# Performance work log

Hardware: AMD Instinct MI355X
Metric: run time of the kernel (lower is better)

Reference implementation:

```python
import jax, jax.numpy as jnp
import numpy as np

S, T, B, V, E, H = 64, 48, 32, 32000, 512, 512


def setup_inputs() -> dict:
    key = jax.random.key(0)
    ks = jax.random.split(key, 24)
    def n(k, shape, s=0.05):
        return jax.random.normal(k, shape, dtype=jnp.float32) * s
    return {
        "src": jax.random.randint(ks[0], (S, B), 0, V),
        "trg": jax.random.randint(ks[1], (T, B), 0, V),
        "enc_emb": n(ks[2], (V, E)),
        "enc_Wih0": n(ks[3], (3 * H, E)),
        "enc_Whh0": n(ks[4], (3 * H, H)),
        "enc_bih0": n(ks[5], (3 * H,)),
        "enc_bhh0": n(ks[6], (3 * H,)),
        "enc_Wih1": n(ks[7], (3 * H, H)),
        "enc_Whh1": n(ks[8], (3 * H, H)),
        "enc_bih1": n(ks[9], (3 * H,)),
        "enc_bhh1": n(ks[10], (3 * H,)),
        "dec_emb": n(ks[11], (V, E)),
        "dec_Wih0": n(ks[12], (3 * H, E)),
        "dec_Whh0": n(ks[13], (3 * H, H)),
        "dec_bih0": n(ks[14], (3 * H,)),
        "dec_bhh0": n(ks[15], (3 * H,)),
        "dec_Wih1": n(ks[16], (3 * H, H)),
        "dec_Whh1": n(ks[17], (3 * H, H)),
        "dec_bih1": n(ks[18], (3 * H,)),
        "dec_bhh1": n(ks[19], (3 * H,)),
        "out_W": n(ks[20], (V, H)),
        "out_b": n(ks[21], (V,)),
    }


def gru_layer(xs, h0, Wih, Whh, bih, bhh):
    """PyTorch-convention GRU over a (T, B, D) sequence. Returns (ys, h_T)."""
    def step(h, x):
        gi = x @ Wih.T + bih          # (B, 3H)
        gh = h @ Whh.T + bhh          # (B, 3H)
        ir, iz, inn = jnp.split(gi, 3, axis=-1)
        hr, hz, hn = jnp.split(gh, 3, axis=-1)
        r = jax.nn.sigmoid(ir + hr)
        z = jax.nn.sigmoid(iz + hz)
        cand = jnp.tanh(inn + r * hn)
        h_new = (1.0 - z) * cand + z * h
        return h_new, h_new
    hT, ys = jax.lax.scan(step, h0, xs)
    return ys, hT


def reference(src, trg, enc_emb, enc_Wih0, enc_Whh0, enc_bih0, enc_bhh0,
              enc_Wih1, enc_Whh1, enc_bih1, enc_bhh1,
              dec_emb, dec_Wih0, dec_Whh0, dec_bih0, dec_bhh0,
              dec_Wih1, dec_Whh1, dec_bih1, dec_bhh1, out_W, out_b):
    b = src.shape[1]
    h = enc_Whh0.shape[1]
    h0 = jnp.zeros((b, h), dtype=enc_emb.dtype)
    # Encoder: 2-layer unidirectional GRU (dropout=0, eval mode)
    x = enc_emb[src]                                   # (S, B, E)
    y0, h0_f = gru_layer(x, h0, enc_Wih0, enc_Whh0, enc_bih0, enc_bhh0)
    _, h1_f = gru_layer(y0, h0, enc_Wih1, enc_Whh1, enc_bih1, enc_bhh1)
    # decoder_hidden = encoder_hidden[-2:] -> (layer0 final, layer1 final)
    # Decoder with teacher_forcing_ratio = 1.0: inputs are trg[:-1]
    d = dec_emb[trg[:-1]]                              # (T-1, B, E)
    d0, _ = gru_layer(d, h0_f, dec_Wih0, dec_Whh0, dec_bih0, dec_bhh0)
    d1, _ = gru_layer(d0, h1_f, dec_Wih1, dec_Whh1, dec_bih1, dec_bhh1)
    logits = d1 @ out_W.T + out_b                      # (T-1, B, V)
    return logits
```

## Files before the change

### kernel.cpp

```cpp
#include <hip/hip_runtime.h>
#include <hip/hip_bf16.h>

typedef __bf16 bf16x8 __attribute__((ext_vector_type(8)));
typedef float  f32x4  __attribute__((ext_vector_type(4)));

__device__ __forceinline__ void store_bf8(__bf16* dst, float4 a, float4 b) {
  bf16x8 v;
  v[0] = (__bf16)a.x; v[1] = (__bf16)a.y; v[2] = (__bf16)a.z; v[3] = (__bf16)a.w;
  v[4] = (__bf16)b.x; v[5] = (__bf16)b.y; v[6] = (__bf16)b.z; v[7] = (__bf16)b.w;
  *(bf16x8*)dst = v;
}

__device__ __forceinline__ bf16x8 load_coh16(const __bf16* p) {
  union { unsigned long long u[2]; bf16x8 v; } r;
  r.u[0] = __hip_atomic_load((const unsigned long long*)p,     __ATOMIC_RELAXED, __HIP_MEMORY_SCOPE_AGENT);
  r.u[1] = __hip_atomic_load((const unsigned long long*)p + 1, __ATOMIC_RELAXED, __HIP_MEMORY_SCOPE_AGENT);
  return r.v;
}

__device__ __forceinline__ void store_coh16B(__bf16* p, bf16x8 v) {
  asm volatile("global_store_dwordx4 %0, %1, off sc0 sc1"
               :: "v"(p), "v"(v) : "memory");
}

__device__ __forceinline__ void wait_flags(const unsigned* f, unsigned tgt) {
  const unsigned* p = f + (threadIdx.x & 31) * 32;
  for (;;) {
    const unsigned v = __hip_atomic_load(p, __ATOMIC_RELAXED, __HIP_MEMORY_SCOPE_AGENT);
    if (__all((int)(v >= tgt))) break;
    __builtin_amdgcn_s_sleep(1);
  }
}

__global__ __launch_bounds__(256) void cvt_f32_bf16(
    const float* __restrict__ s, __bf16* __restrict__ d, long n8)
{
  long i = (long)blockIdx.x * 256 + threadIdx.x;
  if (i >= n8) return;
  const float4* sp = (const float4*)s + i * 2;
  store_bf8(d + i * 8, sp[0], sp[1]);
}

__global__ __launch_bounds__(64) void gather_cvt(
    const float* __restrict__ emb, const int* __restrict__ idx, __bf16* __restrict__ dst)
{
  const int r = blockIdx.x;
  const long row = idx[r];
  const float4* sp = (const float4*)(emb + row * 512) + threadIdx.x * 2;
  store_bf8(dst + (long)r * 512 + threadIdx.x * 8, sp[0], sp[1]);
}

__global__ __launch_bounds__(256) void gemm_bt(
    const __bf16* __restrict__ A, const __bf16* __restrict__ B,
    const float* __restrict__ bias, float* __restrict__ C, int M, int N)
{
  const int wave = threadIdx.x >> 6;
  const int lane = threadIdx.x & 63;
  const int l16 = lane & 15;
  const int quad = lane >> 4;

  const int m0 = blockIdx.x * 128 + wave * 32;
  const int n0 = blockIdx.y * 128;

  int r0 = m0 + l16;       if (r0 >= M) r0 = M - 1;
  int r1 = m0 + 16 + l16;  if (r1 >= M) r1 = M - 1;
  const __bf16* __restrict__ A0 = A + (long)r0 * 512 + quad * 8;
  const __bf16* __restrict__ A1 = A + (long)r1 * 512 + quad * 8;

  const __bf16* bp[8];
#pragma unroll
  for (int i = 0; i < 8; ++i)
    bp[i] = B + (long)(n0 + i * 16 + l16) * 512 + quad * 8;

  f32x4 acc[2][8];
#pragma unroll
  for (int mi = 0; mi < 2; ++mi)
#pragma unroll
    for (int i = 0; i < 8; ++i) acc[mi][i] = (f32x4){0.f, 0.f, 0.f, 0.f};

#pragma unroll
  for (int ks = 0; ks < 16; ++ks) {
    bf16x8 a0 = *(const bf16x8*)(A0 + ks * 32);
    bf16x8 a1 = *(const bf16x8*)(A1 + ks * 32);
#pragma unroll
    for (int i = 0; i < 8; ++i) {
      bf16x8 b = *(const bf16x8*)(bp[i] + ks * 32);
      acc[0][i] = __builtin_amdgcn_mfma_f32_16x16x32_bf16(a0, b, acc[0][i], 0, 0, 0);
      acc[1][i] = __builtin_amdgcn_mfma_f32_16x16x32_bf16(a1, b, acc[1][i], 0, 0, 0);
    }
  }

#pragma unroll
  for (int mi = 0; mi < 2; ++mi) {
    const int crow = m0 + mi * 16 + quad * 4;
#pragma unroll
    for (int i = 0; i < 8; ++i) {
      const int n = n0 + i * 16 + l16;
      const float bv = bias ? bias[n] : 0.0f;
#pragma unroll
      for (int r = 0; r < 4; ++r) {
        const int row = crow + r;
        if (row < M) C[(long)row * N + n] = acc[mi][i][r] + bv;
      }
    }
  }
}

__global__ __launch_bounds__(128) void gru2_pipe(
    const float* __restrict__ GI,
    const float* __restrict__ Whh0, const float* __restrict__ bhh0,
    const float* __restrict__ Wih1, const float* __restrict__ bih1,
    const float* __restrict__ Whh1, const float* __restrict__ bhh1,
    __bf16* __restrict__ Y0, __bf16* __restrict__ Y1,
    const __bf16* __restrict__ h0i, const __bf16* __restrict__ h1i,
    float* __restrict__ hf0, float* __restrict__ hf1,
    unsigned* __restrict__ flags0, unsigned* __restrict__ flags1, int T)
{
  __shared__ __align__(16) __bf16 wh[48 * 520];
  __shared__ __align__(16) __bf16 wi[48 * 520];
  __shared__ __align__(16) __bf16 hlds[32][16];

  const int tid = threadIdx.x;
  const int L   = blockIdx.x >> 5;
  const int c   = blockIdx.x & 31;
  const int w   = tid >> 6;
  const int lane = tid & 63;
  const int l16 = lane & 15;
  const int quad = lane >> 4;

  const float* __restrict__ Whh = L ? Whh1 : Whh0;
  const float* __restrict__ bhh = L ? bhh1 : bhh0;
  __bf16* __restrict__ Yown = L ? Y1 : Y0;
  const __bf16* __restrict__ hini = L ? h1i : h0i;
  float* __restrict__ hf = L ? hf1 : hf0;
  unsigned* __restrict__ fOwn = L ? flags1 : flags0;

  for (int ch = tid; ch < 48 * 64; ch += 128) {
    const int lr = ch >> 6, kc = ch & 63;
    const int g = lr >> 4, j = lr & 15;
    const float4* sp = (const float4*)(Whh + (long)(g * 512 + c * 16 + j) * 512) + kc * 2;
    store_bf8(&wh[lr * 520 + kc * 8], sp[0], sp[1]);
  }
  if (L) {
    for (int ch = tid; ch < 48 * 64; ch += 128) {
      const int lr = ch >> 6, kc = ch & 63;
      const int g = lr >> 4, j = lr & 15;
      const float4* sp = (const float4*)(Wih1 + (long)(g * 512 + c * 16 + j) * 512) + kc * 2;
      store_bf8(&wi[lr * 520 + kc * 8], sp[0], sp[1]);
    }
  }

  float bR = bhh[0 * 512 + c * 16 + l16];
  float bZ = bhh[1 * 512 + c * 16 + l16];
  float bH = bhh[2 * 512 + c * 16 + l16];
  float bN = 0.f;
  if (L) {
    bR += bih1[0 * 512 + c * 16 + l16];
    bZ += bih1[1 * 512 + c * 16 + l16];
    bN  = bih1[2 * 512 + c * 16 + l16];
  }
  __syncthreads();

  const int b0  = w * 16 + quad * 4;
  const int col = c * 16 + l16;

  float hprev[4];
#pragma unroll
  for (int r = 0; r < 4; ++r) hprev[r] = hf[(b0 + r) * 512 + col];

  for (int t = 0; t < T; ++t) {
    float giR[4] = {0, 0, 0, 0}, giZ[4] = {0, 0, 0, 0}, giN[4] = {0, 0, 0, 0};
    if (!L) {
      const float* GIt = GI + (long)t * 49152;
#pragma unroll
      for (int r = 0; r < 4; ++r) {
        const float* gp = GIt + (b0 + r) * 1536 + col;
        giR[r] = gp[0];
        giZ[r] = gp[512];
        giN[r] = gp[1024];
      }
    }

    f32x4 accR = {bR, bR, bR, bR};
    f32x4 accZ = {bZ, bZ, bZ, bZ};
    f32x4 accH = {bH, bH, bH, bH};
    f32x4 accN = {bN, bN, bN, bN};

    if (L) {
      wait_flags(flags0, (unsigned)(t + 1));
      const __bf16* xA = Y0 + (long)(t + 1) * 16384 + (w * 16 + l16) * 512 + quad * 8;
      bf16x8 xa[16];
#pragma unroll
      for (int ks = 0; ks < 16; ++ks) xa[ks] = load_coh16(xA + ks * 32);
#pragma unroll
      for (int ks = 0; ks < 16; ++ks) {
        const int o = ks * 32 + quad * 8;
        accR = __builtin_amdgcn_mfma_f32_16x16x32_bf16(xa[ks], *(const bf16x8*)&wi[(     l16) * 520 + o], accR, 0, 0, 0);
        accZ = __builtin_amdgcn_mfma_f32_16x16x32_bf16(xa[ks], *(const bf16x8*)&wi[(16 + l16) * 520 + o], accZ, 0, 0, 0);
        accN = __builtin_amdgcn_mfma_f32_16x16x32_bf16(xa[ks], *(const bf16x8*)&wi[(32 + l16) * 520 + o], accN, 0, 0, 0);
      }
      if (t) wait_flags(flags1, (unsigned)t);
    } else if (t) {
      wait_flags(flags0, (unsigned)t);
    }

    const __bf16* hsrc = t ? (Yown + (long)t * 16384) : hini;
    const __bf16* hA = hsrc + (w * 16 + l16) * 512 + quad * 8;
    bf16x8 ha[16];
#pragma unroll
    for (int ks = 0; ks < 16; ++ks) ha[ks] = load_coh16(hA + ks * 32);
#pragma unroll
    for (int ks = 0; ks < 16; ++ks) {
      const int o = ks * 32 + quad * 8;
      accR = __builtin_amdgcn_mfma_f32_16x16x32_bf16(ha[ks], *(const bf16x8*)&wh[(     l16) * 520 + o], accR, 0, 0, 0);
      accZ = __builtin_amdgcn_mfma_f32_16x16x32_bf16(ha[ks], *(const bf16x8*)&wh[(16 + l16) * 520 + o], accZ, 0, 0, 0);
      accH = __builtin_amdgcn_mfma_f32_16x16x32_bf16(ha[ks], *(const bf16x8*)&wh[(32 + l16) * 520 + o], accH, 0, 0, 0);
    }

#pragma unroll
    for (int r = 0; r < 4; ++r) {
      float rs = accR[r], zs = accZ[r], hn = accH[r], nn = accN[r];
      if (!L) { rs += giR[r]; zs += giZ[r]; nn = giN[r]; }
      const float rg = __fdividef(1.0f, 1.0f + __expf(-rs));
      const float zg = __fdividef(1.0f, 1.0f + __expf(-zs));
      const float a2 = nn + rg * hn;
      const float e2 = __expf(2.0f * a2);
      const float cand = 1.0f - __fdividef(2.0f, e2 + 1.0f);
      const float hnew = (1.0f - zg) * cand + zg * hprev[r];
      hprev[r] = hnew;
      hlds[b0 + r][l16] = (__bf16)hnew;
    }
    __syncthreads();

    __bf16* yout = Yown + (long)(t + 1) * 16384;
    if (tid < 64) {
      const int row = tid >> 1, half = tid & 1;
      bf16x8 hv = *(const bf16x8*)&hlds[row][half * 8];
      store_coh16B(yout + (long)row * 512 + c * 16 + half * 8, hv);
    }
    asm volatile("s_waitcnt vmcnt(0)" ::: "memory");
    __syncthreads();
    if (tid == 0)
      __hip_atomic_store(fOwn + c * 32, (unsigned)(t + 1),
                         __ATOMIC_RELAXED, __HIP_MEMORY_SCOPE_AGENT);
  }

#pragma unroll
  for (int r = 0; r < 4; ++r) hf[(b0 + r) * 512 + col] = hprev[r];
}

extern "C" void kernel_launch(void* const* d_in, const int* in_sizes, int n_in,
                              void* d_out, int out_size, void* d_ws, size_t ws_size,
                              hipStream_t stream)
{
  const int* src = (const int*)d_in[0];
  const int* trg = (const int*)d_in[1];
  const float* enc_emb  = (const float*)d_in[2];
  const float* enc_Wih0 = (const float*)d_in[3];
  const float* enc_Whh0 = (const float*)d_in[4];
  const float* enc_bih0 = (const float*)d_in[5];
  const float* enc_bhh0 = (const float*)d_in[6];
  const float* enc_Wih1 = (const float*)d_in[7];
  const float* enc_Whh1 = (const float*)d_in[8];
  const float* enc_bih1 = (const float*)d_in[9];
  const float* enc_bhh1 = (const float*)d_in[10];
  const float* dec_emb  = (const float*)d_in[11];
  const float* dec_Wih0 = (const float*)d_in[12];
  const float* dec_Whh0 = (const float*)d_in[13];
  const float* dec_bih0 = (const float*)d_in[14];
  const float* dec_bhh0 = (const float*)d_in[15];
  const float* dec_Wih1 = (const float*)d_in[16];
  const float* dec_Whh1 = (const float*)d_in[17];
  const float* dec_bih1 = (const float*)d_in[18];
  const float* dec_bhh1 = (const float*)d_in[19];
  const float* out_W    = (const float*)d_in[20];
  const float* out_b    = (const float*)d_in[21];

  char* ws = (char*)d_ws;
  float*  GI    = (float*)(ws + 0);
  __bf16* Xenc  = (__bf16*)(ws + 12582912);
  __bf16* Xdec  = (__bf16*)(ws + 14680064);
  __bf16* Y0e   = (__bf16*)(ws + 16220160);
  __bf16* Y1e   = (__bf16*)(ws + 18350080);
  __bf16* Y0d   = (__bf16*)(ws + 20480000);
  __bf16* Y1d   = (__bf16*)(ws + 22052864);
  __bf16* Wb0   = (__bf16*)(ws + 23625728);
  __bf16* Wb2   = (__bf16*)(ws + 25198592);
  __bf16* outWb = (__bf16*)(ws + 26771456);
  float*  hf0   = (float*)(ws + 59539456);
  float*  hf1   = (float*)(ws + 59604992);
  __bf16* zb    = (__bf16*)(ws + 59670528);
  unsigned* flags = (unsigned*)(ws + 59703296);

  hipMemsetAsync(hf0, 0, 131072, stream);
  hipMemsetAsync(zb, 0, 32768, stream);
  hipMemsetAsync(flags, 0, 16384, stream);

  gather_cvt<<<2048, 64, 0, stream>>>(enc_emb, src, Xenc);
  gather_cvt<<<1504, 64, 0, stream>>>(dec_emb, trg, Xdec);
  cvt_f32_bf16<<<384, 256, 0, stream>>>(enc_Wih0, Wb0, 98304);
  cvt_f32_bf16<<<384, 256, 0, stream>>>(dec_Wih0, Wb2, 98304);
  cvt_f32_bf16<<<8000, 256, 0, stream>>>(out_W, outWb, 2048000);

  gemm_bt<<<dim3(16, 12), 256, 0, stream>>>(Xenc, Wb0, enc_bih0, GI, 2048, 1536);
  gru2_pipe<<<64, 128, 0, stream>>>(GI, enc_Whh0, enc_bhh0,
                                    enc_Wih1, enc_bih1, enc_Whh1, enc_bhh1,
                                    Y0e, Y1e, zb, zb, hf0, hf1,
                                    flags + 0, flags + 1024, 64);
  gemm_bt<<<dim3(12, 12), 256, 0, stream>>>(Xdec, Wb2, dec_bih0, GI, 1504, 1536);
  gru2_pipe<<<64, 128, 0, stream>>>(GI, dec_Whh0, dec_bhh0,
                                    dec_Wih1, dec_bih1, dec_Whh1, dec_bhh1,
                                    Y0d, Y1d, Y0e + 64 * 16384, Y1e + 64 * 16384, hf0, hf1,
                                    flags + 2048, flags + 3072, 47);

  gemm_bt<<<dim3(12, 250), 256, 0, stream>>>(Y1d + 16384, outWb, out_b,
                                             (float*)d_out, 1504, 32000);
}
```

Baseline: 1.299 ms.

## Stage GEMM tiles in LDS with swizzle and per-wave GRU sync flags

The GEMM is rewritten to stage 128x64 A/B tiles in shared memory with an XOR swizzle, register prefetch of the next K slab, and a 1-D grid with an XCD-aware block remap. Separately, the GRU pipeline drops block-wide barriers in favour of per-wave flags, so each wave waits only on the matching batch half. Its coherent atomic loads become plain vector loads, and h is stored with per-lane dwordx2. The plain loads after relaxed flag polling may read stale data across workgroups, which risks correctness in exchange for lower sync and load overhead.

New measurement: 1.235 ms. 1.05x faster.

```diff
diff --git a/kernel.cpp b/kernel.cpp
--- a/kernel.cpp
+++ b/kernel.cpp
@@ -11,25 +11,14 @@
   *(bf16x8*)dst = v;
 }
 
-__device__ __forceinline__ bf16x8 load_coh16(const __bf16* p) {
-  union { unsigned long long u[2]; bf16x8 v; } r;
-  r.u[0] = __hip_atomic_load((const unsigned long long*)p,     __ATOMIC_RELAXED, __HIP_MEMORY_SCOPE_AGENT);
-  r.u[1] = __hip_atomic_load((const unsigned long long*)p + 1, __ATOMIC_RELAXED, __HIP_MEMORY_SCOPE_AGENT);
-  return r.v;
-}
-
-__device__ __forceinline__ void store_coh16B(__bf16* p, bf16x8 v) {
-  asm volatile("global_store_dwordx4 %0, %1, off sc0 sc1"
-               :: "v"(p), "v"(v) : "memory");
-}
-
-__device__ __forceinline__ void wait_flags(const unsigned* f, unsigned tgt) {
-  const unsigned* p = f + (threadIdx.x & 31) * 32;
+__device__ __forceinline__ void wait_flags_w(const unsigned* f, int w, unsigned tgt) {
+  const unsigned* p = f + ((((threadIdx.x & 31) << 1) + w) << 5);
   for (;;) {
     const unsigned v = __hip_atomic_load(p, __ATOMIC_RELAXED, __HIP_MEMORY_SCOPE_AGENT);
     if (__all((int)(v >= tgt))) break;
     __builtin_amdgcn_s_sleep(1);
   }
+  asm volatile("" ::: "memory");
 }
 
 __global__ __launch_bounds__(256) void cvt_f32_bf16(
@@ -50,27 +39,38 @@
   store_bf8(dst + (long)r * 512 + threadIdx.x * 8, sp[0], sp[1]);
 }
 
-__global__ __launch_bounds__(256) void gemm_bt(
+__global__ __launch_bounds__(256) void gemm_tile(
     const __bf16* __restrict__ A, const __bf16* __restrict__ B,
-    const float* __restrict__ bias, float* __restrict__ C, int M, int N)
-{
-  const int wave = threadIdx.x >> 6;
-  const int lane = threadIdx.x & 63;
-  const int l16 = lane & 15;
+    const float* __restrict__ bias, float* __restrict__ C,
+    int M, int N, int NT)
+{
+  __shared__ __align__(16) __bf16 sA[128 * 64];
+  __shared__ __align__(16) __bf16 sB[128 * 64];
+
+  const int nwg = gridDim.x;
+  const int bid = blockIdx.x;
+  const int swz = (nwg & 7) ? bid : ((bid & 7) * (nwg >> 3) + (bid >> 3));
+  const int m0 = (swz / NT) * 128;
+  const int n0 = (swz % NT) * 128;
+
+  const int tid  = threadIdx.x;
+  const int wave = tid >> 6;
+  const int lane = tid & 63;
+  const int l16  = lane & 15;
   const int quad = lane >> 4;
 
-  const int m0 = blockIdx.x * 128 + wave * 32;
-  const int n0 = blockIdx.y * 128;
-
-  int r0 = m0 + l16;       if (r0 >= M) r0 = M - 1;
-  int r1 = m0 + 16 + l16;  if (r1 >= M) r1 = M - 1;
-  const __bf16* __restrict__ A0 = A + (long)r0 * 512 + quad * 8;
-  const __bf16* __restrict__ A1 = A + (long)r1 * 512 + quad * 8;
-
-  const __bf16* bp[8];
-#pragma unroll
-  for (int i = 0; i < 8; ++i)
-    bp[i] = B + (long)(n0 + i * 16 + l16) * 512 + quad * 8;
+  int srow[4], sch[4];
+  const __bf16* ga[4];
+  const __bf16* gb[4];
+#pragma unroll
+  for (int s = 0; s < 4; ++s) {
+    const int e = s * 256 + tid;
+    srow[s] = e >> 3;
+    sch[s]  = e & 7;
+    int ra = m0 + srow[s]; if (ra >= M) ra = M - 1;
+    ga[s] = A + (long)ra * 512 + sch[s] * 8;
+    gb[s] = B + (long)(n0 + srow[s]) * 512 + sch[s] * 8;
+  }
 
   f32x4 acc[2][8];
 #pragma unroll
@@ -78,21 +78,47 @@
 #pragma unroll
     for (int i = 0; i < 8; ++i) acc[mi][i] = (f32x4){0.f, 0.f, 0.f, 0.f};
 
-#pragma unroll
-  for (int ks = 0; ks < 16; ++ks) {
-    bf16x8 a0 = *(const bf16x8*)(A0 + ks * 32);
-    bf16x8 a1 = *(const bf16x8*)(A1 + ks * 32);
-#pragma unroll
-    for (int i = 0; i < 8; ++i) {
-      bf16x8 b = *(const bf16x8*)(bp[i] + ks * 32);
-      acc[0][i] = __builtin_amdgcn_mfma_f32_16x16x32_bf16(a0, b, acc[0][i], 0, 0, 0);
-      acc[1][i] = __builtin_amdgcn_mfma_f32_16x16x32_bf16(a1, b, acc[1][i], 0, 0, 0);
+  bf16x8 aval[4], bval[4];
+#pragma unroll
+  for (int s = 0; s < 4; ++s) {
+    aval[s] = *(const bf16x8*)(ga[s]);
+    bval[s] = *(const bf16x8*)(gb[s]);
+  }
+
+  for (int k0 = 0; k0 < 512; k0 += 64) {
+    __syncthreads();
+#pragma unroll
+    for (int s = 0; s < 4; ++s) {
+      const int slot = (sch[s] ^ (srow[s] & 7)) << 3;
+      *(bf16x8*)&sA[srow[s] * 64 + slot] = aval[s];
+      *(bf16x8*)&sB[srow[s] * 64 + slot] = bval[s];
+    }
+    if (k0 + 64 < 512) {
+#pragma unroll
+      for (int s = 0; s < 4; ++s) {
+        aval[s] = *(const bf16x8*)(ga[s] + k0 + 64);
+        bval[s] = *(const bf16x8*)(gb[s] + k0 + 64);
+      }
+    }
+    __syncthreads();
+
+#pragma unroll
+    for (int ks = 0; ks < 2; ++ks) {
+      const int ck = (((ks * 4 + quad) ^ (l16 & 7)) << 3);
+      bf16x8 a0 = *(const bf16x8*)&sA[(wave * 32 +      l16) * 64 + ck];
+      bf16x8 a1 = *(const bf16x8*)&sA[(wave * 32 + 16 + l16) * 64 + ck];
+#pragma unroll
+      for (int i = 0; i < 8; ++i) {
+        bf16x8 b = *(const bf16x8*)&sB[(i * 16 + l16) * 64 + ck];
+        acc[0][i] = __builtin_amdgcn_mfma_f32_16x16x32_bf16(a0, b, acc[0][i], 0, 0, 0);
+        acc[1][i] = __builtin_amdgcn_mfma_f32_16x16x32_bf16(a1, b, acc[1][i], 0, 0, 0);
+      }
     }
   }
 
 #pragma unroll
   for (int mi = 0; mi < 2; ++mi) {
-    const int crow = m0 + mi * 16 + quad * 4;
+    const int crow = m0 + wave * 32 + mi * 16 + quad * 4;
 #pragma unroll
     for (int i = 0; i < 8; ++i) {
       const int n = n0 + i * 16 + l16;
@@ -163,6 +189,8 @@
 
   const int b0  = w * 16 + quad * 4;
   const int col = c * 16 + l16;
+  const int srow = w * 16 + (lane >> 2);
+  const int sch4 = (lane & 3) * 4;
 
   float hprev[4];
 #pragma unroll
@@ -187,11 +215,11 @@
     f32x4 accN = {bN, bN, bN, bN};
 
     if (L) {
-      wait_flags(flags0, (unsigned)(t + 1));
+      wait_flags_w(flags0, w, (unsigned)(t + 1));
       const __bf16* xA = Y0 + (long)(t + 1) * 16384 + (w * 16 + l16) * 512 + quad * 8;
       bf16x8 xa[16];
 #pragma unroll
-      for (int ks = 0; ks < 16; ++ks) xa[ks] = load_coh16(xA + ks * 32);
+      for (int ks = 0; ks < 16; ++ks) xa[ks] = *(const bf16x8*)(xA + ks * 32);
 #pragma unroll
       for (int ks = 0; ks < 16; ++ks) {
         const int o = ks * 32 + quad * 8;
@@ -199,16 +227,16 @@
         accZ = __builtin_amdgcn_mfma_f32_16x16x32_bf16(xa[ks], *(const bf16x8*)&wi[(16 + l16) * 520 + o], accZ, 0, 0, 0);
         accN = __builtin_amdgcn_mfma_f32_16x16x32_bf16(xa[ks], *(const bf16x8*)&wi[(32 + l16) * 520 + o], accN, 0, 0, 0);
       }
-      if (t) wait_flags(flags1, (unsigned)t);
+      if (t) wait_flags_w(flags1, w, (unsigned)t);
     } else if (t) {
-      wait_flags(flags0, (unsigned)t);
+      wait_flags_w(flags0, w, (unsigned)t);
     }
 
     const __bf16* hsrc = t ? (Yown + (long)t * 16384) : hini;
     const __bf16* hA = hsrc + (w * 16 + l16) * 512 + quad * 8;
     bf16x8 ha[16];
 #pragma unroll
-    for (int ks = 0; ks < 16; ++ks) ha[ks] = load_coh16(hA + ks * 32);
+    for (int ks = 0; ks < 16; ++ks) ha[ks] = *(const bf16x8*)(hA + ks * 32);
 #pragma unroll
     for (int ks = 0; ks < 16; ++ks) {
       const int o = ks * 32 + quad * 8;
@@ -230,18 +258,18 @@
       hprev[r] = hnew;
       hlds[b0 + r][l16] = (__bf16)hnew;
     }
-    __syncthreads();
+    asm volatile("" ::: "memory");
 
     __bf16* yout = Yown + (long)(t + 1) * 16384;
-    if (tid < 64) {
-      const int row = tid >> 1, half = tid & 1;
-      bf16x8 hv = *(const bf16x8*)&hlds[row][half * 8];
-      store_coh16B(yout + (long)row * 512 + c * 16 + half * 8, hv);
+    {
+      unsigned long long pv = *(const unsigned long long*)&hlds[srow][sch4];
+      __bf16* dst = yout + (long)srow * 512 + c * 16 + sch4;
+      asm volatile("global_store_dwordx2 %0, %1, off sc0 sc1"
+                   :: "v"(dst), "v"(pv) : "memory");
     }
     asm volatile("s_waitcnt vmcnt(0)" ::: "memory");
-    __syncthreads();
-    if (tid == 0)
-      __hip_atomic_store(fOwn + c * 32, (unsigned)(t + 1),
+    if (lane == 0)
+      __hip_atomic_store(fOwn + (((c << 1) + w) << 5), (unsigned)(t + 1),
                          __ATOMIC_RELAXED, __HIP_MEMORY_SCOPE_AGENT);
   }
 
@@ -294,7 +322,7 @@
 
   hipMemsetAsync(hf0, 0, 131072, stream);
   hipMemsetAsync(zb, 0, 32768, stream);
-  hipMemsetAsync(flags, 0, 16384, stream);
+  hipMemsetAsync(flags, 0, 32768, stream);
 
   gather_cvt<<<2048, 64, 0, stream>>>(enc_emb, src, Xenc);
   gather_cvt<<<1504, 64, 0, stream>>>(dec_emb, trg, Xdec);
@@ -302,17 +330,17 @@
   cvt_f32_bf16<<<384, 256, 0, stream>>>(dec_Wih0, Wb2, 98304);
   cvt_f32_bf16<<<8000, 256, 0, stream>>>(out_W, outWb, 2048000);
 
-  gemm_bt<<<dim3(16, 12), 256, 0, stream>>>(Xenc, Wb0, enc_bih0, GI, 2048, 1536);
+  gemm_tile<<<192, 256, 0, stream>>>(Xenc, Wb0, enc_bih0, GI, 2048, 1536, 12);
   gru2_pipe<<<64, 128, 0, stream>>>(GI, enc_Whh0, enc_bhh0,
                                     enc_Wih1, enc_bih1, enc_Whh1, enc_bhh1,
                                     Y0e, Y1e, zb, zb, hf0, hf1,
-                                    flags + 0, flags + 1024, 64);
-  gemm_bt<<<dim3(12, 12), 256, 0, stream>>>(Xdec, Wb2, dec_bih0, GI, 1504, 1536);
+                                    flags + 0, flags + 2048, 64);
+  gemm_tile<<<144, 256, 0, stream>>>(Xdec, Wb2, dec_bih0, GI, 1504, 1536, 12);
   gru2_pipe<<<64, 128, 0, stream>>>(GI, dec_Whh0, dec_bhh0,
                                     dec_Wih1, dec_bih1, dec_Whh1, dec_bhh1,
                                     Y0d, Y1d, Y0e + 64 * 16384, Y1e + 64 * 16384, hf0, hf1,
-                                    flags + 2048, flags + 3072, 47);
-
-  gemm_bt<<<dim3(12, 250), 256, 0, stream>>>(Y1d + 16384, outWb, out_b,
-                                             (float*)d_out, 1504, 32000);
-}
+                                    flags + 4096, flags + 6144, 47);
+
+  gemm_tile<<<3000, 256, 0, stream>>>(Y1d + 16384, outWb, out_b,
+                                      (float*)d_out, 1504, 32000, 250);
+}
```
